# Kernel optimization log

Measured on AMD Instinct MI355X. Metric: run time of the kernel, lower is better.

The kernel has to match this reference:

```python
import jax, jax.numpy as jnp
import numpy as np

GRID_SIZE = 3
SPLINE_ORDER = 3
N_BASIS = GRID_SIZE + SPLINE_ORDER  # 6


def make_grid(in_features, dtype=jnp.float32):
    # efficient-kan grid buffer: extended uniform knots over grid_range=[-1, 1]
    h = 2.0 / GRID_SIZE
    g = jnp.arange(-SPLINE_ORDER, GRID_SIZE + SPLINE_ORDER + 1, dtype=dtype) * h - 1.0
    return jnp.tile(g[None, :], (in_features, 1))  # (in, G + 2S + 1)


def b_splines(x, grid):
    # x: (N, in), grid: (in, G+2S+1) -> (N, in, G+S) via Cox-de Boor recursion
    xb = x[..., None]
    bases = ((xb >= grid[:, :-1]) & (xb < grid[:, 1:])).astype(x.dtype)
    for k in range(1, SPLINE_ORDER + 1):
        bases = ((xb - grid[:, : -(k + 1)]) / (grid[:, k:-1] - grid[:, : -(k + 1)]) * bases[..., :-1]
                 + (grid[:, k + 1:] - xb) / (grid[:, k + 1:] - grid[:, 1:-k]) * bases[..., 1:])
    return bases


def kan_linear(x, base_w, spline_w, scaler, grid):
    # base path: silu(x) @ W_base^T ; spline path: contraction of basis with scaled spline weights
    base = jax.nn.silu(x) @ base_w.T
    scaled_sw = spline_w * scaler[..., None]  # (out, in, K)
    spl = jnp.einsum('nik,oik->no', b_splines(x, grid), scaled_sw)
    return base + spl


def setup_inputs() -> dict:
    key = jax.random.key(0)
    ks = jax.random.split(key, 7)
    B, C, P, D, H = 8, 8, 128, 256, 1024
    s = 0.05
    return {
        'x': jax.random.normal(ks[0], (B, C, P, D), dtype=jnp.float32),
        'base_w1': s * jax.random.normal(ks[1], (H, D), dtype=jnp.float32),
        'spline_w1': s * jax.random.normal(ks[2], (H, D, N_BASIS), dtype=jnp.float32),
        'scaler1': 1.0 + s * jax.random.normal(ks[3], (H, D), dtype=jnp.float32),
        'base_w2': s * jax.random.normal(ks[4], (D, H), dtype=jnp.float32),
        'spline_w2': s * jax.random.normal(ks[5], (D, H, N_BASIS), dtype=jnp.float32),
        'scaler2': 1.0 + s * jax.random.normal(ks[6], (D, H), dtype=jnp.float32),
    }


def reference(x, base_w1, spline_w1, scaler1, base_w2, spline_w2, scaler2):
    B, C, P, D = x.shape
    H = base_w1.shape[0]
    xf = x.reshape(-1, D)  # KANLinear flattens leading dims to tokens
    g1 = make_grid(D, x.dtype)
    g2 = make_grid(H, x.dtype)
    h = kan_linear(xf, base_w1, spline_w1, scaler1, g1)
    h = jax.nn.gelu(h, approximate=False)  # torch F.gelu default = exact erf
    # dropout is identity in eval / with p used as inference baseline
    y = kan_linear(h, base_w2, spline_w2, scaler2, g2)
    return y.reshape(B, C, P, D)
```

## Files before the change

### kernel.cpp

```cpp
#include <hip/hip_runtime.h>
#include <hip/hip_bf16.h>
#include <math.h>


typedef __attribute__((ext_vector_type(8))) short bf16x8;
typedef __attribute__((ext_vector_type(4))) float f32x4;

#define TOKENS 8192
#define D_IN   256
#define D_HID  1024

__device__ __forceinline__ void kan_features(float x, float f[8]) {
    f[0] = x * __builtin_amdgcn_rcpf(1.0f + __expf(-x));
    const float s = (x + 1.0f) * 1.5f + 3.0f;
    const float cf = floorf(s);
    const float u = s - cf;
    const int c = (int)cf;
    const float u2 = u * u, u3 = u2 * u;
    const float k6 = 1.0f / 6.0f;
    const float v3 = u3 * k6;
    const float v2 = (-3.0f * u3 + 3.0f * u2 + 3.0f * u + 1.0f) * k6;
    const float v1 = (3.0f * u3 - 6.0f * u2 + 4.0f) * k6;
    const float w1 = 1.0f - u;
    const float v0 = w1 * w1 * w1 * k6;
    const bool in = (s >= 0.0f) && (s < 9.0f);
#pragma unroll
    for (int j = 0; j < 6; ++j) {
        int d = c - j;
        float bv = (d == 0) ? v3 : (d == 1) ? v2 : (d == 2) ? v1 : (d == 3) ? v0 : 0.0f;
        f[1 + j] = in ? bv : 0.0f;
    }
    f[7] = 0.0f;
}

__device__ __forceinline__ void features_to_bf16(const float f[8], __hip_bfloat16 fb[8]) {
#pragma unroll
    for (int j = 0; j < 8; ++j) fb[j] = __float2bfloat16(f[j]);
}

__global__ void init_fused(const float* __restrict__ X, __hip_bfloat16* __restrict__ F,
                           const float* __restrict__ bw1, const float* __restrict__ sw1,
                           const float* __restrict__ sc1, __hip_bfloat16* __restrict__ W1,
                           const float* __restrict__ bw2, const float* __restrict__ sw2,
                           const float* __restrict__ sc2, __hip_bfloat16* __restrict__ W2) {
    const int b = blockIdx.x;
    if (b < 8192) {
        int idx = b * 256 + threadIdx.x;
        float f[8];
        kan_features(X[idx], f);
        __hip_bfloat16 fb[8];
        features_to_bf16(f, fb);
        *(bf16x8*)&F[(size_t)idx * 8] = *(bf16x8*)fb;
        return;
    }
    const bool w1 = (b < 9216);
    int idx = (w1 ? (b - 8192) : (b - 9216)) * 256 + threadIdx.x;
    const float* bw = w1 ? bw1 : bw2;
    const float* sw = w1 ? sw1 : sw2;
    const float* sc = w1 ? sc1 : sc2;
    __hip_bfloat16* Wo = w1 ? W1 : W2;
    float scl = sc[idx];
    __hip_bfloat16 row[8];
    row[0] = __float2bfloat16(bw[idx]);
#pragma unroll
    for (int j = 0; j < 6; ++j)
        row[1 + j] = __float2bfloat16(sw[idx * 6 + j] * scl);
    row[7] = __float2bfloat16(0.0f);
    *(bf16x8*)&Wo[(size_t)idx * 8] = *(bf16x8*)row;
}

#define GLL(src, dst) __builtin_amdgcn_global_load_lds(                         \
    (const __attribute__((address_space(1))) void*)(src),                       \
    (__attribute__((address_space(3))) void*)(dst), 16, 0, 0)

__global__ __launch_bounds__(256, 2)
void kan_gemm1(const __hip_bfloat16* __restrict__ A,
               const __hip_bfloat16* __restrict__ W,
               float* __restrict__ H) {
    constexpr int K = D_IN * 8;
    constexpr int NT = K / 64;
    __shared__ __hip_bfloat16 Al[2][128 * 64];
    __shared__ __hip_bfloat16 Bl[2][128 * 64];

    const int tid = threadIdx.x;
    const int wid = tid >> 6, lane = tid & 63;
    const int wm = wid >> 1, wn = wid & 1;
    const int lr = lane & 15, lg = lane >> 4;
    const int n0 = blockIdx.x * 128, o0 = blockIdx.y * 128;

    int srow[4], sslot[4];
#pragma unroll
    for (int p = 0; p < 4; ++p) {
        int item = tid + p * 256;
        srow[p] = item >> 3;
        sslot[p] = (item & 7) ^ (srow[p] & 7);
    }
    int aoff[2][4], boff[2][4];
#pragma unroll
    for (int ks = 0; ks < 2; ++ks)
#pragma unroll
        for (int f = 0; f < 4; ++f) {
            int ar = wm * 64 + f * 16 + lr;
            int br = wn * 64 + f * 16 + lr;
            aoff[ks][f] = ar * 64 + (((ks * 4 + lg) ^ (ar & 7)) * 8);
            boff[ks][f] = br * 64 + (((ks * 4 + lg) ^ (br & 7)) * 8);
        }

    f32x4 acc[4][4] = {};

#define STG1(buf, kt)                                                           \
    do {                                                                        \
        _Pragma("unroll")                                                       \
        for (int p = 0; p < 4; ++p) {                                           \
            GLL(A + (size_t)(n0 + srow[p]) * K + (kt) * 64 + sslot[p] * 8,      \
                &Al[buf][(tid + p * 256) * 8]);                                 \
            GLL(W + (size_t)(o0 + srow[p]) * K + (kt) * 64 + sslot[p] * 8,      \
                &Bl[buf][(tid + p * 256) * 8]);                                 \
        }                                                                       \
    } while (0)

    STG1(0, 0);
    STG1(1, 1);
    for (int t = 0; t < NT; ++t) {
        const int cur = t & 1;
        asm volatile("s_waitcnt vmcnt(8)" ::: "memory");
        __builtin_amdgcn_s_barrier();
        __builtin_amdgcn_sched_barrier(0);
#pragma unroll
        for (int ks = 0; ks < 2; ++ks) {
            bf16x8 af[4], bfr[4];
#pragma unroll
            for (int f = 0; f < 4; ++f) af[f] = *(const bf16x8*)&Al[cur][aoff[ks][f]];
#pragma unroll
            for (int f = 0; f < 4; ++f) bfr[f] = *(const bf16x8*)&Bl[cur][boff[ks][f]];
#pragma unroll
            for (int fm = 0; fm < 4; ++fm)
#pragma unroll
                for (int fn = 0; fn < 4; ++fn)
                    acc[fm][fn] = __builtin_amdgcn_mfma_f32_16x16x32_bf16(
                        af[fm], bfr[fn], acc[fm][fn], 0, 0, 0);
        }
        asm volatile("s_waitcnt lgkmcnt(0)" ::: "memory");
        __builtin_amdgcn_s_barrier();
        __builtin_amdgcn_sched_barrier(0);
        const int kn = (t + 2 < NT) ? t + 2 : NT - 1;
        STG1(cur, kn);
    }
#undef STG1
#pragma unroll
    for (int fm = 0; fm < 4; ++fm) {
#pragma unroll
        for (int fn = 0; fn < 4; ++fn) {
            int col = o0 + wn * 64 + fn * 16 + lr;
#pragma unroll
            for (int r = 0; r < 4; ++r) {
                int row = n0 + wm * 64 + fm * 16 + lg * 4 + r;
                float v = acc[fm][fn][r];
                H[(size_t)row * D_HID + col] = 0.5f * v * (1.0f + erff(v * 0.70710678118f));
            }
        }
    }
}

__global__ __launch_bounds__(256, 5)
void kan_gemm2(const float* __restrict__ H,
               const __hip_bfloat16* __restrict__ W,
               float* __restrict__ P) {
    constexpr int OUT = D_IN, KD = D_HID * 8;
    constexpr int NTT = KD / 32;
    __shared__ __hip_bfloat16 Al[64 * 32];
    __shared__ __hip_bfloat16 Bl[256 * 32];

    const int tid = threadIdx.x;
    const int wid = tid >> 6, lane = tid & 63;
    const int lr = lane & 15, lg = lane >> 4;
    const int n0 = blockIdx.x * 64;

    const int per = NTT / 8;
    const int ks0 = blockIdx.z * per, ks1 = ks0 + per;

    int srow[4], sslot[4];
#pragma unroll
    for (int p = 0; p < 4; ++p) {
        int item = tid + p * 256;
        srow[p] = item >> 2;
        sslot[p] = (item & 3) ^ (srow[p] & 3);
    }
    const int frow = tid >> 2, fc = tid & 3;
    const float* hp = H + (size_t)(n0 + frow) * D_HID + fc;
    const int aw = frow * 32 + ((fc ^ (frow & 3)) * 8);

    int aoff[4], boff[4];
#pragma unroll
    for (int f = 0; f < 4; ++f) {
        int ar = f * 16 + lr;
        int br = wid * 64 + f * 16 + lr;
        aoff[f] = ar * 32 + ((lg ^ (ar & 3)) * 8);
        boff[f] = br * 32 + ((lg ^ (br & 3)) * 8);
    }

    f32x4 acc[4][4] = {};

    float hv = hp[(size_t)ks0 * 4];
    for (int kt = ks0; kt < ks1; ++kt) {
        float hc = hv;
        const int knext = (kt + 1 < ks1) ? kt + 1 : ks1 - 1;
        hv = hp[(size_t)knext * 4];
        {
            float ff[8]; __hip_bfloat16 fb[8];
            kan_features(hc, ff); features_to_bf16(ff, fb);
            *(bf16x8*)&Al[aw] = *(bf16x8*)fb;
        }
#pragma unroll
        for (int p = 0; p < 4; ++p)
            GLL(W + (size_t)srow[p] * KD + (size_t)kt * 32 + sslot[p] * 8,
                &Bl[(tid + p * 256) * 8]);
        __syncthreads();
        bf16x8 af[4], bfr[4];
#pragma unroll
        for (int f = 0; f < 4; ++f) af[f] = *(const bf16x8*)&Al[aoff[f]];
#pragma unroll
        for (int f = 0; f < 4; ++f) bfr[f] = *(const bf16x8*)&Bl[boff[f]];
#pragma unroll
        for (int fm = 0; fm < 4; ++fm)
#pragma unroll
            for (int fn = 0; fn < 4; ++fn)
                acc[fm][fn] = __builtin_amdgcn_mfma_f32_16x16x32_bf16(
                    af[fm], bfr[fn], acc[fm][fn], 0, 0, 0);
        __syncthreads();
    }

    float* Pl = (float*)Bl;
    const size_t zoff = (size_t)blockIdx.z * TOKENS * OUT;
#pragma unroll
    for (int q = 0; q < 4; ++q) {
        __syncthreads();
        if (wid == q) {
#pragma unroll
            for (int fm = 0; fm < 4; ++fm)
#pragma unroll
                for (int fn = 0; fn < 4; ++fn)
#pragma unroll
                    for (int r = 0; r < 4; ++r)
                        Pl[(fm * 16 + lg * 4 + r) * 64 + fn * 16 + lr] = acc[fm][fn][r];
        }
        __syncthreads();
#pragma unroll
        for (int p = 0; p < 4; ++p) {
            int v = tid + p * 256;
            int row = v >> 4, cv = (v & 15) * 4;
            *(f32x4*)&P[zoff + (size_t)(n0 + row) * OUT + q * 64 + cv] =
                *(const f32x4*)&Pl[row * 64 + cv];
        }
    }
}

__global__ void reduce_split(const float* __restrict__ P, float* __restrict__ out,
                             int nvec) {
    int i = blockIdx.x * 256 + threadIdx.x;
    if (i >= nvec) return;
    const f32x4* Pv = (const f32x4*)P;
    f32x4 s = Pv[i];
#pragma unroll
    for (int z = 1; z < 8; ++z) s += Pv[(size_t)z * nvec + i];
    ((f32x4*)out)[i] = s;
}

extern "C" void kernel_launch(void* const* d_in, const int* in_sizes, int n_in,
                              void* d_out, int out_size, void* d_ws, size_t ws_size,
                              hipStream_t stream) {
    const float* x   = (const float*)d_in[0];
    const float* bw1 = (const float*)d_in[1];
    const float* sw1 = (const float*)d_in[2];
    const float* sc1 = (const float*)d_in[3];
    const float* bw2 = (const float*)d_in[4];
    const float* sw2 = (const float*)d_in[5];
    const float* sc2 = (const float*)d_in[6];
    float* out = (float*)d_out;

    char* ws = (char*)d_ws;
    __hip_bfloat16* W1 = (__hip_bfloat16*)ws;
    __hip_bfloat16* W2 = (__hip_bfloat16*)(ws + (4ull << 20));
    __hip_bfloat16* F1 = (__hip_bfloat16*)(ws + (8ull << 20));
    float*          Hb = (float*)(ws + (40ull << 20));
    float*          Pp = (float*)(ws + (72ull << 20));

    if (ws_size < (136ull << 20)) return;

    init_fused<<<10240, 256, 0, stream>>>(x, F1, bw1, sw1, sc1, W1, bw2, sw2, sc2, W2);

    kan_gemm1<<<dim3(TOKENS / 128, D_HID / 128), 256, 0, stream>>>(F1, W1, Hb);

    kan_gemm2<<<dim3(TOKENS / 64, 1, 8), 256, 0, stream>>>(Hb, W2, Pp);

    const int nvec = TOKENS * D_IN / 4;
    reduce_split<<<(nvec + 255) / 256, 256, 0, stream>>>(Pp, out, nvec);
}
```

Measured before the change: 152.9 us.

## Retile second KAN GEMM to 64x128 tiles with K=64 steps; prioritize MFMA in GEMM1

The second GEMM now splits the 256 output columns across two blocks (128 each). Each K step covers 64 instead of 32, and the four waves are arranged as a 2x2 grid with 32x64 tiles each. This halves barrier count per K and raises the grid size, at the cost of computing the spline features of each hidden activation twice (once per output half). GEMM1 also raises wave priority around its MFMA section using s_setprio. Launch bounds for GEMM2 are raised to 6 waves per SIMD.

```diff
diff --git a/kernel.cpp b/kernel.cpp
--- a/kernel.cpp
+++ b/kernel.cpp
@@ -126,6 +126,7 @@
         asm volatile("s_waitcnt vmcnt(8)" ::: "memory");
         __builtin_amdgcn_s_barrier();
         __builtin_amdgcn_sched_barrier(0);
+        __builtin_amdgcn_s_setprio(1);
 #pragma unroll
         for (int ks = 0; ks < 2; ++ks) {
             bf16x8 af[4], bfr[4];
@@ -140,6 +141,7 @@
                     acc[fm][fn] = __builtin_amdgcn_mfma_f32_16x16x32_bf16(
                         af[fm], bfr[fn], acc[fm][fn], 0, 0, 0);
         }
+        __builtin_amdgcn_s_setprio(0);
         asm volatile("s_waitcnt lgkmcnt(0)" ::: "memory");
         __builtin_amdgcn_s_barrier();
         __builtin_amdgcn_sched_barrier(0);
@@ -162,19 +164,21 @@
     }
 }
 
-__global__ __launch_bounds__(256, 5)
+__global__ __launch_bounds__(256, 6)
 void kan_gemm2(const float* __restrict__ H,
                const __hip_bfloat16* __restrict__ W,
                float* __restrict__ P) {
     constexpr int OUT = D_IN, KD = D_HID * 8;
-    constexpr int NTT = KD / 32;
-    __shared__ __hip_bfloat16 Al[64 * 32];
-    __shared__ __hip_bfloat16 Bl[256 * 32];
+    constexpr int NTT = KD / 64;
+    __shared__ __hip_bfloat16 Al[64 * 64];
+    __shared__ __hip_bfloat16 Bl[128 * 64];
 
     const int tid = threadIdx.x;
     const int wid = tid >> 6, lane = tid & 63;
+    const int wm = wid >> 1, wn = wid & 1;
     const int lr = lane & 15, lg = lane >> 4;
     const int n0 = blockIdx.x * 64;
+    const int o0 = blockIdx.y * 128;
 
     const int per = NTT / 8;
     const int ks0 = blockIdx.z * per, ks1 = ks0 + per;
@@ -183,73 +187,90 @@
 #pragma unroll
     for (int p = 0; p < 4; ++p) {
         int item = tid + p * 256;
-        srow[p] = item >> 2;
-        sslot[p] = (item & 3) ^ (srow[p] & 3);
-    }
-    const int frow = tid >> 2, fc = tid & 3;
-    const float* hp = H + (size_t)(n0 + frow) * D_HID + fc;
-    const int aw = frow * 32 + ((fc ^ (frow & 3)) * 8);
-
-    int aoff[4], boff[4];
-#pragma unroll
-    for (int f = 0; f < 4; ++f) {
-        int ar = f * 16 + lr;
-        int br = wid * 64 + f * 16 + lr;
-        aoff[f] = ar * 32 + ((lg ^ (ar & 3)) * 8);
-        boff[f] = br * 32 + ((lg ^ (br & 3)) * 8);
-    }
-
-    f32x4 acc[4][4] = {};
-
-    float hv = hp[(size_t)ks0 * 4];
+        srow[p] = item >> 3;
+        sslot[p] = (item & 7) ^ (srow[p] & 7);
+    }
+    const int ar0 = tid >> 3, ac = tid & 7;
+    const float* hp0 = H + (size_t)(n0 + ar0) * D_HID + ac;
+    const float* hp1 = H + (size_t)(n0 + ar0 + 32) * D_HID + ac;
+    const int aw0 = ar0 * 64 + ((ac ^ (ar0 & 7)) * 8);
+    const int aw1 = (ar0 + 32) * 64 + ((ac ^ ((ar0 + 32) & 7)) * 8);
+
+    int aoff[2][2], boff[2][4];
+#pragma unroll
+    for (int ks = 0; ks < 2; ++ks) {
+#pragma unroll
+        for (int f = 0; f < 2; ++f) {
+            int ar = wm * 32 + f * 16 + lr;
+            aoff[ks][f] = ar * 64 + (((ks * 4 + lg) ^ (ar & 7)) * 8);
+        }
+#pragma unroll
+        for (int f = 0; f < 4; ++f) {
+            int br = wn * 64 + f * 16 + lr;
+            boff[ks][f] = br * 64 + (((ks * 4 + lg) ^ (br & 7)) * 8);
+        }
+    }
+
+    f32x4 acc[2][4] = {};
+
+    float hv0 = hp0[(size_t)ks0 * 8];
+    float hv1 = hp1[(size_t)ks0 * 8];
+
     for (int kt = ks0; kt < ks1; ++kt) {
-        float hc = hv;
+#pragma unroll
+        for (int p = 0; p < 4; ++p)
+            GLL(W + (size_t)(o0 + srow[p]) * KD + (size_t)kt * 64 + sslot[p] * 8,
+                &Bl[(tid + p * 256) * 8]);
+        float hc0 = hv0, hc1 = hv1;
         const int knext = (kt + 1 < ks1) ? kt + 1 : ks1 - 1;
-        hv = hp[(size_t)knext * 4];
+        hv0 = hp0[(size_t)knext * 8];
+        hv1 = hp1[(size_t)knext * 8];
         {
             float ff[8]; __hip_bfloat16 fb[8];
-            kan_features(hc, ff); features_to_bf16(ff, fb);
-            *(bf16x8*)&Al[aw] = *(bf16x8*)fb;
-        }
-#pragma unroll
-        for (int p = 0; p < 4; ++p)
-            GLL(W + (size_t)srow[p] * KD + (size_t)kt * 32 + sslot[p] * 8,
-                &Bl[(tid + p * 256) * 8]);
+            kan_features(hc0, ff); features_to_bf16(ff, fb);
+            *(bf16x8*)&Al[aw0] = *(bf16x8*)fb;
+            kan_features(hc1, ff); features_to_bf16(ff, fb);
+            *(bf16x8*)&Al[aw1] = *(bf16x8*)fb;
+        }
         __syncthreads();
-        bf16x8 af[4], bfr[4];
-#pragma unroll
-        for (int f = 0; f < 4; ++f) af[f] = *(const bf16x8*)&Al[aoff[f]];
-#pragma unroll
-        for (int f = 0; f < 4; ++f) bfr[f] = *(const bf16x8*)&Bl[boff[f]];
-#pragma unroll
-        for (int fm = 0; fm < 4; ++fm)
-#pragma unroll
-            for (int fn = 0; fn < 4; ++fn)
-                acc[fm][fn] = __builtin_amdgcn_mfma_f32_16x16x32_bf16(
-                    af[fm], bfr[fn], acc[fm][fn], 0, 0, 0);
+#pragma unroll
+        for (int ks = 0; ks < 2; ++ks) {
+            bf16x8 af[2], bfr[4];
+#pragma unroll
+            for (int f = 0; f < 2; ++f) af[f] = *(const bf16x8*)&Al[aoff[ks][f]];
+#pragma unroll
+            for (int f = 0; f < 4; ++f) bfr[f] = *(const bf16x8*)&Bl[boff[ks][f]];
+#pragma unroll
+            for (int fm = 0; fm < 2; ++fm)
+#pragma unroll
+                for (int fn = 0; fn < 4; ++fn)
+                    acc[fm][fn] = __builtin_amdgcn_mfma_f32_16x16x32_bf16(
+                        af[fm], bfr[fn], acc[fm][fn], 0, 0, 0);
+        }
         __syncthreads();
     }
 
     float* Pl = (float*)Bl;
     const size_t zoff = (size_t)blockIdx.z * TOKENS * OUT;
 #pragma unroll
-    for (int q = 0; q < 4; ++q) {
+    for (int h = 0; h < 2; ++h) {
         __syncthreads();
-        if (wid == q) {
-#pragma unroll
-            for (int fm = 0; fm < 4; ++fm)
+        if (wn == h) {
+#pragma unroll
+            for (int fm = 0; fm < 2; ++fm)
 #pragma unroll
                 for (int fn = 0; fn < 4; ++fn)
 #pragma unroll
                     for (int r = 0; r < 4; ++r)
-                        Pl[(fm * 16 + lg * 4 + r) * 64 + fn * 16 + lr] = acc[fm][fn][r];
+                        Pl[(wm * 32 + fm * 16 + lg * 4 + r) * 64 + fn * 16 + lr] =
+                            acc[fm][fn][r];
         }
         __syncthreads();
 #pragma unroll
         for (int p = 0; p < 4; ++p) {
             int v = tid + p * 256;
             int row = v >> 4, cv = (v & 15) * 4;
-            *(f32x4*)&P[zoff + (size_t)(n0 + row) * OUT + q * 64 + cv] =
+            *(f32x4*)&P[zoff + (size_t)(n0 + row) * OUT + o0 + h * 64 + cv] =
                 *(const f32x4*)&Pl[row * 64 + cv];
         }
     }
@@ -291,7 +312,7 @@
 
     kan_gemm1<<<dim3(TOKENS / 128, D_HID / 128), 256, 0, stream>>>(F1, W1, Hb);
 
-    kan_gemm2<<<dim3(TOKENS / 64, 1, 8), 256, 0, stream>>>(Hb, W2, Pp);
+    kan_gemm2<<<dim3(TOKENS / 64, 2, 8), 256, 0, stream>>>(Hb, W2, Pp);
 
     const int nvec = TOKENS * D_IN / 4;
     reduce_split<<<(nvec + 255) / 256, 256, 0, stream>>>(Pp, out, nvec);
```

Result: slower. 163.7 us (+7.0%).

## Pre-swizzle W2 into MFMA fragment layout and load B directly from global in gemm2

Applied to the files above, without the earlier changes.

The init kernel now writes the second-layer weights in a fragment-ordered layout, so gemm2 can load B operands straight from global memory into registers instead of staging them through LDS. gemm2 switches to a 64-wide K step with a double-buffered LDS tile holding only the on-the-fly spline features, and overlaps feature generation for the next tile with the current MFMAs. s_setprio is raised around the MFMA sections in both GEMMs. In exchange, occupancy is lowered (launch bounds 5 to 3), and the direct global B loads rely on cache hits and latency hiding across waves.

```diff
diff --git a/kernel.cpp b/kernel.cpp
--- a/kernel.cpp
+++ b/kernel.cpp
@@ -42,7 +42,7 @@
                            const float* __restrict__ bw1, const float* __restrict__ sw1,
                            const float* __restrict__ sc1, __hip_bfloat16* __restrict__ W1,
                            const float* __restrict__ bw2, const float* __restrict__ sw2,
-                           const float* __restrict__ sc2, __hip_bfloat16* __restrict__ W2) {
+                           const float* __restrict__ sc2, __hip_bfloat16* __restrict__ W2f) {
     const int b = blockIdx.x;
     if (b < 8192) {
         int idx = b * 256 + threadIdx.x;
@@ -58,7 +58,6 @@
     const float* bw = w1 ? bw1 : bw2;
     const float* sw = w1 ? sw1 : sw2;
     const float* sc = w1 ? sc1 : sc2;
-    __hip_bfloat16* Wo = w1 ? W1 : W2;
     float scl = sc[idx];
     __hip_bfloat16 row[8];
     row[0] = __float2bfloat16(bw[idx]);
@@ -66,7 +65,12 @@
     for (int j = 0; j < 6; ++j)
         row[1 + j] = __float2bfloat16(sw[idx * 6 + j] * scl);
     row[7] = __float2bfloat16(0.0f);
-    *(bf16x8*)&Wo[(size_t)idx * 8] = *(bf16x8*)row;
+    if (w1) {
+        *(bf16x8*)&W1[(size_t)idx * 8] = *(bf16x8*)row;
+    } else {
+        int o = idx >> 10, i = idx & 1023;
+        *(bf16x8*)&W2f[(size_t)(i >> 2) * 8192 + o * 32 + (i & 3) * 8] = *(bf16x8*)row;
+    }
 }
 
 #define GLL(src, dst) __builtin_amdgcn_global_load_lds(                         \
@@ -126,6 +130,7 @@
         asm volatile("s_waitcnt vmcnt(8)" ::: "memory");
         __builtin_amdgcn_s_barrier();
         __builtin_amdgcn_sched_barrier(0);
+        __builtin_amdgcn_s_setprio(1);
 #pragma unroll
         for (int ks = 0; ks < 2; ++ks) {
             bf16x8 af[4], bfr[4];
@@ -140,6 +145,7 @@
                     acc[fm][fn] = __builtin_amdgcn_mfma_f32_16x16x32_bf16(
                         af[fm], bfr[fn], acc[fm][fn], 0, 0, 0);
         }
+        __builtin_amdgcn_s_setprio(0);
         asm volatile("s_waitcnt lgkmcnt(0)" ::: "memory");
         __builtin_amdgcn_s_barrier();
         __builtin_amdgcn_sched_barrier(0);
@@ -162,14 +168,13 @@
     }
 }
 
-__global__ __launch_bounds__(256, 5)
+__global__ __launch_bounds__(256, 3)
 void kan_gemm2(const float* __restrict__ H,
-               const __hip_bfloat16* __restrict__ W,
+               const __hip_bfloat16* __restrict__ W2f,
                float* __restrict__ P) {
     constexpr int OUT = D_IN, KD = D_HID * 8;
-    constexpr int NTT = KD / 32;
-    __shared__ __hip_bfloat16 Al[64 * 32];
-    __shared__ __hip_bfloat16 Bl[256 * 32];
+    constexpr int NTT = KD / 64;
+    __shared__ __hip_bfloat16 Al[2][64 * 64];
 
     const int tid = threadIdx.x;
     const int wid = tid >> 6, lane = tid & 63;
@@ -179,58 +184,89 @@
     const int per = NTT / 8;
     const int ks0 = blockIdx.z * per, ks1 = ks0 + per;
 
-    int srow[4], sslot[4];
-#pragma unroll
-    for (int p = 0; p < 4; ++p) {
-        int item = tid + p * 256;
-        srow[p] = item >> 2;
-        sslot[p] = (item & 3) ^ (srow[p] & 3);
-    }
-    const int frow = tid >> 2, fc = tid & 3;
-    const float* hp = H + (size_t)(n0 + frow) * D_HID + fc;
-    const int aw = frow * 32 + ((fc ^ (frow & 3)) * 8);
-
-    int aoff[4], boff[4];
-#pragma unroll
-    for (int f = 0; f < 4; ++f) {
-        int ar = f * 16 + lr;
-        int br = wid * 64 + f * 16 + lr;
-        aoff[f] = ar * 32 + ((lg ^ (ar & 3)) * 8);
-        boff[f] = br * 32 + ((lg ^ (br & 3)) * 8);
-    }
+    const int ar0 = tid >> 3, ac = tid & 7;
+    const float* hp0 = H + (size_t)(n0 + ar0) * D_HID + ac;
+    const float* hp1 = H + (size_t)(n0 + ar0 + 32) * D_HID + ac;
+    const int aw0 = ar0 * 64 + ((ac ^ (ar0 & 7)) * 8);
+    const int aw1 = (ar0 + 32) * 64 + ((ac ^ ((ar0 + 32) & 7)) * 8);
+
+    int bcol[4];
+#pragma unroll
+    for (int f = 0; f < 4; ++f)
+        bcol[f] = (wid * 64 + f * 16 + lr) * 32 + lg * 8;
+
+    int aoff[2][4];
+#pragma unroll
+    for (int ks = 0; ks < 2; ++ks)
+#pragma unroll
+        for (int f = 0; f < 4; ++f) {
+            int ar = f * 16 + lr;
+            aoff[ks][f] = ar * 64 + (((ks * 4 + lg) ^ (ar & 7)) * 8);
+        }
 
     f32x4 acc[4][4] = {};
 
-    float hv = hp[(size_t)ks0 * 4];
-    for (int kt = ks0; kt < ks1; ++kt) {
-        float hc = hv;
-        const int knext = (kt + 1 < ks1) ? kt + 1 : ks1 - 1;
-        hv = hp[(size_t)knext * 4];
-        {
-            float ff[8]; __hip_bfloat16 fb[8];
-            kan_features(hc, ff); features_to_bf16(ff, fb);
-            *(bf16x8*)&Al[aw] = *(bf16x8*)fb;
-        }
-#pragma unroll
-        for (int p = 0; p < 4; ++p)
-            GLL(W + (size_t)srow[p] * KD + (size_t)kt * 32 + sslot[p] * 8,
-                &Bl[(tid + p * 256) * 8]);
-        __syncthreads();
-        bf16x8 af[4], bfr[4];
-#pragma unroll
-        for (int f = 0; f < 4; ++f) af[f] = *(const bf16x8*)&Al[aoff[f]];
-#pragma unroll
-        for (int f = 0; f < 4; ++f) bfr[f] = *(const bf16x8*)&Bl[boff[f]];
-#pragma unroll
-        for (int fm = 0; fm < 4; ++fm)
-#pragma unroll
-            for (int fn = 0; fn < 4; ++fn)
-                acc[fm][fn] = __builtin_amdgcn_mfma_f32_16x16x32_bf16(
-                    af[fm], bfr[fn], acc[fm][fn], 0, 0, 0);
-        __syncthreads();
-    }
-
-    float* Pl = (float*)Bl;
+#define FEAT(buf, h0, h1)                                                       \
+    do {                                                                        \
+        float ff[8]; __hip_bfloat16 fb[8];                                      \
+        kan_features(h0, ff); features_to_bf16(ff, fb);                         \
+        *(bf16x8*)&Al[buf][aw0] = *(bf16x8*)fb;                                 \
+        kan_features(h1, ff); features_to_bf16(ff, fb);                         \
+        *(bf16x8*)&Al[buf][aw1] = *(bf16x8*)fb;                                 \
+    } while (0)
+
+#define SUB(T, b, nb, DO_STAGE)                                                 \
+    do {                                                                        \
+        bf16x8 bw[2][4];                                                        \
+        _Pragma("unroll")                                                       \
+        for (int ks = 0; ks < 2; ++ks)                                          \
+            _Pragma("unroll")                                                   \
+            for (int f = 0; f < 4; ++f)                                         \
+                bw[ks][f] = *(const bf16x8*)&W2f[(size_t)((T) * 2 + ks) * 8192  \
+                                                 + bcol[f]];                    \
+        if (DO_STAGE) {                                                         \
+            FEAT(nb, hA, hB);                                                   \
+            int hn = ((T) + 2 < ks1) ? (T) + 2 : ks1 - 1;                       \
+            hA = hp0[(size_t)hn * 8];                                           \
+            hB = hp1[(size_t)hn * 8];                                           \
+        }                                                                       \
+        asm volatile("s_waitcnt lgkmcnt(0)" ::: "memory");                      \
+        __builtin_amdgcn_sched_barrier(0);                                      \
+        __builtin_amdgcn_s_barrier();                                           \
+        __builtin_amdgcn_s_setprio(1);                                          \
+        _Pragma("unroll")                                                       \
+        for (int ks = 0; ks < 2; ++ks) {                                        \
+            bf16x8 af[4];                                                       \
+            _Pragma("unroll")                                                   \
+            for (int f = 0; f < 4; ++f)                                         \
+                af[f] = *(const bf16x8*)&Al[b][aoff[ks][f]];                    \
+            _Pragma("unroll")                                                   \
+            for (int fm = 0; fm < 4; ++fm)                                      \
+                _Pragma("unroll")                                               \
+                for (int fn = 0; fn < 4; ++fn)                                  \
+                    acc[fm][fn] = __builtin_amdgcn_mfma_f32_16x16x32_bf16(      \
+                        af[fm], bw[ks][fn], acc[fm][fn], 0, 0, 0);              \
+        }                                                                       \
+        __builtin_amdgcn_s_setprio(0);                                          \
+        __builtin_amdgcn_s_barrier();                                           \
+    } while (0)
+
+    {
+        float h0 = hp0[(size_t)ks0 * 8];
+        float h1 = hp1[(size_t)ks0 * 8];
+        FEAT(0, h0, h1);
+    }
+    float hA = hp0[(size_t)(ks0 + 1) * 8];
+    float hB = hp1[(size_t)(ks0 + 1) * 8];
+
+    for (int t = ks0; t < ks1; t += 2) {
+        SUB(t, 0, 1, 1);
+        SUB(t + 1, 1, 0, (t + 2 < ks1));
+    }
+#undef SUB
+#undef FEAT
+
+    float* Pl = (float*)Al;
     const size_t zoff = (size_t)blockIdx.z * TOKENS * OUT;
 #pragma unroll
     for (int q = 0; q < 4; ++q) {
@@ -279,19 +315,19 @@
     float* out = (float*)d_out;
 
     char* ws = (char*)d_ws;
-    __hip_bfloat16* W1 = (__hip_bfloat16*)ws;
-    __hip_bfloat16* W2 = (__hip_bfloat16*)(ws + (4ull << 20));
-    __hip_bfloat16* F1 = (__hip_bfloat16*)(ws + (8ull << 20));
-    float*          Hb = (float*)(ws + (40ull << 20));
-    float*          Pp = (float*)(ws + (72ull << 20));
+    __hip_bfloat16* W1  = (__hip_bfloat16*)ws;
+    __hip_bfloat16* W2f = (__hip_bfloat16*)(ws + (4ull << 20));
+    __hip_bfloat16* F1  = (__hip_bfloat16*)(ws + (8ull << 20));
+    float*          Hb  = (float*)(ws + (40ull << 20));
+    float*          Pp  = (float*)(ws + (72ull << 20));
 
     if (ws_size < (136ull << 20)) return;
 
-    init_fused<<<10240, 256, 0, stream>>>(x, F1, bw1, sw1, sc1, W1, bw2, sw2, sc2, W2);
+    init_fused<<<10240, 256, 0, stream>>>(x, F1, bw1, sw1, sc1, W1, bw2, sw2, sc2, W2f);
 
     kan_gemm1<<<dim3(TOKENS / 128, D_HID / 128), 256, 0, stream>>>(F1, W1, Hb);
 
-    kan_gemm2<<<dim3(TOKENS / 64, 1, 8), 256, 0, stream>>>(Hb, W2, Pp);
+    kan_gemm2<<<dim3(TOKENS / 64, 1, 8), 256, 0, stream>>>(Hb, W2f, Pp);
 
     const int nvec = TOKENS * D_IN / 4;
     reduce_split<<<(nvec + 255) / 256, 256, 0, stream>>>(Pp, out, nvec);
```

Measured after the change: 148.1 us. 1.03x faster.
